# Kernel optimization log

Hardware: AMD Instinct MI355X
Metric: run time of the kernel (lower is better)

The kernel has to match this reference:

```python
import jax, jax.numpy as jnp
import numpy as np

B, M, N = 262144, 3, 256   # batch, soil layers, runoff features
H1, H2 = 256, 128          # MLP hidden widths (layer_units[:-1]); last layer is scalar


def setup_inputs() -> dict:
    key = jax.random.key(0)
    ks = jax.random.split(key, 9)
    runoff = jax.random.uniform(ks[0], (B, M, N), dtype=jnp.float32)
    last_flow = jax.random.uniform(ks[1], (B, M), dtype=jnp.float32)
    last_free_water = jax.random.uniform(ks[2], (B, M), dtype=jnp.float32)
    s = 0.05
    # m independent tiny MLPs, stacked along leading axis m
    W1 = jax.random.normal(ks[3], (M, N, H1), dtype=jnp.float32) * s
    b1 = jnp.zeros((M, H1), dtype=jnp.float32)
    W2 = jax.random.normal(ks[4], (M, H1, H2), dtype=jnp.float32) * s
    b2 = jnp.zeros((M, H2), dtype=jnp.float32)
    W3 = jax.random.normal(ks[5], (M, H2), dtype=jnp.float32) * s  # last layer has 1 unit
    b3 = jnp.zeros((M,), dtype=jnp.float32)
    return {
        "last_flow": last_flow,
        "last_free_water": last_free_water,
        "runoff": runoff,
        "W1": W1, "b1": b1, "W2": W2, "b2": b2, "W3": W3, "b3": b3,
    }


def reference(last_flow, last_free_water, runoff, W1, b1, W2, b2, W3, b3):
    # step 1: add summed runoff to free-water state  (B, M)
    free_water = last_free_water + jnp.sum(runoff, axis=-1)
    # step 2: m small MLPs -> per-layer outflow ratio in (0,1), batched over m via einsum
    a1 = jax.nn.relu(jnp.einsum('bmn,mnh->bmh', runoff, W1) + b1)        # (B, M, H1)
    a2 = jax.nn.relu(jnp.einsum('bmh,mhk->bmk', a1, W2) + b2)            # (B, M, H2)
    ratio = jax.nn.sigmoid(jnp.einsum('bmk,mk->bm', a2, W3) + b3)        # (B, M)
    # step 3: blend free water with previous flow
    flow = free_water * ratio + last_flow * (1.0 - ratio)
    # step 4: update free-water state
    new_free_water = free_water - flow
    return (new_free_water, flow)
```

## Files before the change

kernel.cpp:

```cpp
#include <hip/hip_runtime.h>
#include <hip/hip_bf16.h>


#define B_TOT 262144
#define M_    3
#define N_    256
#define H1_   256
#define H2_   128
#define BM_   (B_TOT * M_)

typedef __bf16 bf16_t;
typedef __bf16  bf16x8 __attribute__((ext_vector_type(8)));
typedef float   f32x16 __attribute__((ext_vector_type(16)));
typedef float   f32x4  __attribute__((ext_vector_type(4)));

__device__ __forceinline__ unsigned pack_bf2(float lo, float hi) {
  union { bf16_t b; unsigned short u; } a, c;
  a.b = (bf16_t)lo; c.b = (bf16_t)hi;
  return ((unsigned)c.u << 16) | (unsigned)a.u;
}

__device__ __forceinline__ void gload_lds16(const void* g, void* l) {
  __builtin_amdgcn_global_load_lds(
      (const __attribute__((address_space(1))) void*)g,
      (__attribute__((address_space(3))) void*)l, 16, 0, 0);
}

__global__ __launch_bounds__(256) void prep_weights(
    const float* __restrict__ W1, const float* __restrict__ W2,
    bf16_t* __restrict__ w1s, bf16_t* __restrict__ w2s)
{
  int id = blockIdx.x * 256 + threadIdx.x;
  const int NW1 = M_ * 16 * 8 * 64;
  const int NW2 = M_ * 16 * 4 * 64;
  if (id < NW1) {
    int lane = id & 63;
    int t    = (id >> 6) & 7;
    int kk   = (id >> 9) & 15;
    int m    = id >> 13;
    int h  = 32 * t + (lane & 31);
    int n0 = 16 * kk + 8 * (lane >> 5);
    bf16x8 v;
#pragma unroll
    for (int ii = 0; ii < 8; ++ii)
      v[ii] = (bf16_t)W1[((size_t)m * N_ + (n0 + ii)) * H1_ + h];
    *reinterpret_cast<bf16x8*>(&w1s[(size_t)id * 8]) = v;
  } else if (id < NW1 + NW2) {
    int j    = id - NW1;
    int lane = j & 63;
    int t2   = (j >> 6) & 3;
    int kk2  = (j >> 8) & 15;
    int m    = j >> 12;
    int k2 = 32 * t2 + (lane & 31);
    int h0 = 16 * kk2 + 8 * (lane >> 5);
    bf16x8 v;
#pragma unroll
    for (int ii = 0; ii < 8; ++ii)
      v[ii] = (bf16_t)W2[((size_t)m * H1_ + (h0 + ii)) * H2_ + k2];
    *reinterpret_cast<bf16x8*>(&w2s[(size_t)j * 8]) = v;
  }
}

__global__ __launch_bounds__(256, 2) void reservoir_kernel(
    const float* __restrict__ last_flow,
    const float* __restrict__ last_fw,
    const float* __restrict__ runoff,
    const float* __restrict__ b1,
    const float* __restrict__ b2,
    const float* __restrict__ W3,
    const float* __restrict__ b3,
    const bf16_t* __restrict__ w1s,
    const bf16_t* __restrict__ w2s,
    float* __restrict__ out)
{
  __shared__ alignas(16) bf16_t sW1[2][4096];
  __shared__ alignas(16) bf16_t sW2[2][2048];
  __shared__ alignas(16) float  sB1[H1_];
  __shared__ alignas(16) float  sB2[H2_];
  __shared__ alignas(16) float  sW3[H2_];

  const int tid  = threadIdx.x;
  const int lane = tid & 63;
  const int wv   = tid >> 6;
  const int m    = blockIdx.y;
  const int hi   = lane >> 5;
  const int r    = lane & 31;
  const int row  = blockIdx.x * 128 + wv * 32 + r;

  const bf16_t* w1base = w1s + (size_t)m * 65536;
  const bf16_t* w2base = w2s + (size_t)m * 32768;

  auto stage_w1 = [&](int kk, int buf) {
#pragma unroll
    for (int c = 0; c < 2; ++c) {
      int chunk = wv * 2 + c;
      gload_lds16(w1base + (size_t)kk * 4096 + chunk * 512 + lane * 8,
                  &sW1[buf][chunk * 512]);
    }
  };
  auto stage_w2 = [&](int kk2, int buf) {
    gload_lds16(w2base + (size_t)kk2 * 2048 + wv * 512 + lane * 8,
                &sW2[buf][wv * 512]);
  };

  if (tid < H1_) sB1[tid] = b1[m * H1_ + tid];
  if (tid < H2_) { sB2[tid] = b2[m * H2_ + tid]; sW3[tid] = W3[m * H2_ + tid]; }
  stage_w1(0, 0);
  __syncthreads();

  f32x16 acc1[8];
#pragma unroll
  for (int t = 0; t < 8; ++t) {
#pragma unroll
    for (int g2 = 0; g2 < 4; ++g2) {
      f32x4 bv = *reinterpret_cast<const f32x4*>(&sB1[32 * t + 8 * g2 + 4 * hi]);
      acc1[t][4 * g2 + 0] = bv[0];
      acc1[t][4 * g2 + 1] = bv[1];
      acc1[t][4 * g2 + 2] = bv[2];
      acc1[t][4 * g2 + 3] = bv[3];
    }
  }

  float rsum = 0.f;
  const float* rowptr = runoff + ((size_t)row * M_ + m) * N_;

#pragma unroll
  for (int kk = 0; kk < 16; ++kk) {
    const int cb = kk & 1;
    if (kk < 15) stage_w1(kk + 1, cb ^ 1);
    else         stage_w2(0, 0);

    f32x4 qa = *reinterpret_cast<const f32x4*>(&rowptr[16 * kk + 8 * hi]);
    f32x4 qb = *reinterpret_cast<const f32x4*>(&rowptr[16 * kk + 8 * hi + 4]);
    rsum += qa[0] + qa[1] + qa[2] + qa[3] + qb[0] + qb[1] + qb[2] + qb[3];
    bf16x8 bfrag;
    bfrag[0] = (bf16_t)qa[0]; bfrag[1] = (bf16_t)qa[1];
    bfrag[2] = (bf16_t)qa[2]; bfrag[3] = (bf16_t)qa[3];
    bfrag[4] = (bf16_t)qb[0]; bfrag[5] = (bf16_t)qb[1];
    bfrag[6] = (bf16_t)qb[2]; bfrag[7] = (bf16_t)qb[3];

#pragma unroll
    for (int t = 0; t < 8; ++t) {
      bf16x8 afrag = *reinterpret_cast<const bf16x8*>(&sW1[cb][t * 512 + lane * 8]);
      acc1[t] = __builtin_amdgcn_mfma_f32_32x32x16_bf16(afrag, bfrag, acc1[t], 0, 0, 0);
    }
    __syncthreads();
  }

  unsigned P[8][2][2][2];
#pragma unroll
  for (int t = 0; t < 8; ++t)
#pragma unroll
    for (int q = 0; q < 2; ++q)
#pragma unroll
      for (int v = 0; v < 2; ++v)
#pragma unroll
        for (int s = 0; s < 2; ++s) {
          int e = 8 * q + 4 * v + 2 * s;
          P[t][q][v][s] = pack_bf2(fmaxf(acc1[t][e], 0.f),
                                   fmaxf(acc1[t][e + 1], 0.f));
        }

  f32x16 acc2[4];
#pragma unroll
  for (int t2 = 0; t2 < 4; ++t2) {
#pragma unroll
    for (int g2 = 0; g2 < 4; ++g2) {
      f32x4 bv = *reinterpret_cast<const f32x4*>(&sB2[32 * t2 + 8 * g2 + 4 * hi]);
      acc2[t2][4 * g2 + 0] = bv[0];
      acc2[t2][4 * g2 + 1] = bv[1];
      acc2[t2][4 * g2 + 2] = bv[2];
      acc2[t2][4 * g2 + 3] = bv[3];
    }
  }

#pragma unroll
  for (int kk2 = 0; kk2 < 16; ++kk2) {
    const int cb = kk2 & 1;
    if (kk2 < 15) stage_w2(kk2 + 1, cb ^ 1);
    const int t = kk2 >> 1, q = kk2 & 1;

    auto r0 = __builtin_amdgcn_permlane32_swap(P[t][q][0][0], P[t][q][1][0], false, false);
    auto r1 = __builtin_amdgcn_permlane32_swap(P[t][q][0][1], P[t][q][1][1], false, false);
    union { unsigned u[4]; bf16x8 v; } bb;
    bb.u[0] = r0[0]; bb.u[1] = r1[0]; bb.u[2] = r0[1]; bb.u[3] = r1[1];

#pragma unroll
    for (int t2 = 0; t2 < 4; ++t2) {
      bf16x8 afrag = *reinterpret_cast<const bf16x8*>(&sW2[cb][t2 * 512 + lane * 8]);
      acc2[t2] = __builtin_amdgcn_mfma_f32_32x32x16_bf16(afrag, bb.v, acc2[t2], 0, 0, 0);
    }
    __syncthreads();
  }

  float part = 0.f;
#pragma unroll
  for (int t2 = 0; t2 < 4; ++t2) {
#pragma unroll
    for (int g2 = 0; g2 < 4; ++g2) {
      f32x4 w3v = *reinterpret_cast<const f32x4*>(&sW3[32 * t2 + 8 * g2 + 4 * hi]);
      part += fmaxf(acc2[t2][4 * g2 + 0], 0.f) * w3v[0]
            + fmaxf(acc2[t2][4 * g2 + 1], 0.f) * w3v[1]
            + fmaxf(acc2[t2][4 * g2 + 2], 0.f) * w3v[2]
            + fmaxf(acc2[t2][4 * g2 + 3], 0.f) * w3v[3];
    }
  }
  part += __shfl_xor(part, 32, 64);
  rsum += __shfl_xor(rsum, 32, 64);

  const float x     = part + b3[m];
  const float ratio = 1.0f / (1.0f + __expf(-x));
  const size_t oi   = (size_t)row * M_ + m;
  const float fw    = last_fw[oi] + rsum;
  const float lf    = last_flow[oi];
  const float flow  = fw * ratio + lf * (1.0f - ratio);
  if (hi == 0) {
    out[oi]        = fw - flow;
    out[BM_ + oi]  = flow;
  }
}

extern "C" void kernel_launch(void* const* d_in, const int* in_sizes, int n_in,
                              void* d_out, int out_size, void* d_ws, size_t ws_size,
                              hipStream_t stream) {
  const float* last_flow = (const float*)d_in[0];
  const float* last_fw   = (const float*)d_in[1];
  const float* runoff    = (const float*)d_in[2];
  const float* W1 = (const float*)d_in[3];
  const float* b1 = (const float*)d_in[4];
  const float* W2 = (const float*)d_in[5];
  const float* b2 = (const float*)d_in[6];
  const float* W3 = (const float*)d_in[7];
  const float* b3 = (const float*)d_in[8];
  float* out = (float*)d_out;

  bf16_t* w1s = (bf16_t*)d_ws;
  bf16_t* w2s = w1s + (size_t)M_ * 65536;

  prep_weights<<<144, 256, 0, stream>>>(W1, W2, w1s, w2s);

  dim3 grid(B_TOT / 128, M_);
  reservoir_kernel<<<grid, 256, 0, stream>>>(last_flow, last_fw, runoff,
                                             b1, b2, W3, b3, w1s, w2s, out);
}
```

Before: 326.8 us.

## Stage runoff tiles through swizzled LDS with async loads and double buffering

Runoff rows are now fetched with global_load_lds into a double-buffered, XOR-swizzled LDS tile, 32 columns per stage, instead of each lane doing direct strided global loads per k-step. W1 staging is widened to two k-steps per stage, halving the number of barriers in layer 1. This is meant to coalesce runoff reads, overlap them with MFMA work and cut synchronisation. The cost is roughly 64KB of LDS per block, which may reduce occupancy below the two blocks per CU requested by the launch bounds.

```diff
diff --git a/kernel.cpp b/kernel.cpp
--- a/kernel.cpp
+++ b/kernel.cpp
@@ -73,7 +73,8 @@
     const bf16_t* __restrict__ w2s,
     float* __restrict__ out)
 {
-  __shared__ alignas(16) bf16_t sW1[2][4096];
+  __shared__ alignas(16) float  sR[2][128 * 32];
+  __shared__ alignas(16) bf16_t sW1[2][8192];
   __shared__ alignas(16) bf16_t sW2[2][2048];
   __shared__ alignas(16) float  sB1[H1_];
   __shared__ alignas(16) float  sB2[H2_];
@@ -85,16 +86,30 @@
   const int m    = blockIdx.y;
   const int hi   = lane >> 5;
   const int r    = lane & 31;
-  const int row  = blockIdx.x * 128 + wv * 32 + r;
+  const int r7   = r & 7;
+  const int row0 = blockIdx.x * 128;
+  const int row  = row0 + wv * 32 + r;
+
+  const int l3 = lane >> 3;
+  const int gsw = (lane & 7) ^ l3;
 
   const bf16_t* w1base = w1s + (size_t)m * 65536;
   const bf16_t* w2base = w2s + (size_t)m * 32768;
 
-  auto stage_w1 = [&](int kk, int buf) {
-#pragma unroll
-    for (int c = 0; c < 2; ++c) {
-      int chunk = wv * 2 + c;
-      gload_lds16(w1base + (size_t)kk * 4096 + chunk * 512 + lane * 8,
+  auto stage_R = [&](int g, int buf) {
+#pragma unroll
+    for (int c = 0; c < 4; ++c) {
+      int slab = wv * 4 + c;
+      const float* src = runoff
+          + ((size_t)(row0 + slab * 8 + l3) * M_ + m) * N_ + 32 * g + 4 * gsw;
+      gload_lds16(src, &sR[buf][slab * 256]);
+    }
+  };
+  auto stage_w1g = [&](int g, int buf) {
+#pragma unroll
+    for (int c = 0; c < 4; ++c) {
+      int chunk = wv * 4 + c;
+      gload_lds16(w1base + (size_t)g * 8192 + chunk * 512 + lane * 8,
                   &sW1[buf][chunk * 512]);
     }
   };
@@ -103,9 +118,10 @@
                 &sW2[buf][wv * 512]);
   };
 
-  if (tid < H1_) sB1[tid] = b1[m * H1_ + tid];
+  sB1[tid] = b1[m * H1_ + tid];
   if (tid < H2_) { sB2[tid] = b2[m * H2_ + tid]; sW3[tid] = W3[m * H2_ + tid]; }
-  stage_w1(0, 0);
+  stage_R(0, 0);
+  stage_w1g(0, 0);
   __syncthreads();
 
   f32x16 acc1[8];
@@ -122,27 +138,32 @@
   }
 
   float rsum = 0.f;
-  const float* rowptr = runoff + ((size_t)row * M_ + m) * N_;
-
-#pragma unroll
-  for (int kk = 0; kk < 16; ++kk) {
-    const int cb = kk & 1;
-    if (kk < 15) stage_w1(kk + 1, cb ^ 1);
-    else         stage_w2(0, 0);
-
-    f32x4 qa = *reinterpret_cast<const f32x4*>(&rowptr[16 * kk + 8 * hi]);
-    f32x4 qb = *reinterpret_cast<const f32x4*>(&rowptr[16 * kk + 8 * hi + 4]);
-    rsum += qa[0] + qa[1] + qa[2] + qa[3] + qb[0] + qb[1] + qb[2] + qb[3];
-    bf16x8 bfrag;
-    bfrag[0] = (bf16_t)qa[0]; bfrag[1] = (bf16_t)qa[1];
-    bfrag[2] = (bf16_t)qa[2]; bfrag[3] = (bf16_t)qa[3];
-    bfrag[4] = (bf16_t)qb[0]; bfrag[5] = (bf16_t)qb[1];
-    bfrag[6] = (bf16_t)qb[2]; bfrag[7] = (bf16_t)qb[3];
-
-#pragma unroll
-    for (int t = 0; t < 8; ++t) {
-      bf16x8 afrag = *reinterpret_cast<const bf16x8*>(&sW1[cb][t * 512 + lane * 8]);
-      acc1[t] = __builtin_amdgcn_mfma_f32_32x32x16_bf16(afrag, bfrag, acc1[t], 0, 0, 0);
+  const float* rrow_base_off = nullptr; (void)rrow_base_off;
+
+#pragma unroll
+  for (int g = 0; g < 8; ++g) {
+    const int cb = g & 1;
+    if (g < 7) { stage_R(g + 1, cb ^ 1); stage_w1g(g + 1, cb ^ 1); }
+    else       { stage_w2(0, 0); }
+
+#pragma unroll
+    for (int q = 0; q < 2; ++q) {
+      const float* rb = &sR[cb][(wv * 32 + r) * 32];
+      f32x4 qa = *reinterpret_cast<const f32x4*>(&rb[((4 * q + 2 * hi + 0) ^ r7) * 4]);
+      f32x4 qb = *reinterpret_cast<const f32x4*>(&rb[((4 * q + 2 * hi + 1) ^ r7) * 4]);
+      rsum += qa[0] + qa[1] + qa[2] + qa[3] + qb[0] + qb[1] + qb[2] + qb[3];
+      bf16x8 bfrag;
+      bfrag[0] = (bf16_t)qa[0]; bfrag[1] = (bf16_t)qa[1];
+      bfrag[2] = (bf16_t)qa[2]; bfrag[3] = (bf16_t)qa[3];
+      bfrag[4] = (bf16_t)qb[0]; bfrag[5] = (bf16_t)qb[1];
+      bfrag[6] = (bf16_t)qb[2]; bfrag[7] = (bf16_t)qb[3];
+
+#pragma unroll
+      for (int t = 0; t < 8; ++t) {
+        bf16x8 afrag = *reinterpret_cast<const bf16x8*>(
+            &sW1[cb][q * 4096 + t * 512 + lane * 8]);
+        acc1[t] = __builtin_amdgcn_mfma_f32_32x32x16_bf16(afrag, bfrag, acc1[t], 0, 0, 0);
+      }
     }
     __syncthreads();
   }
@@ -187,7 +208,8 @@
 
 #pragma unroll
     for (int t2 = 0; t2 < 4; ++t2) {
-      bf16x8 afrag = *reinterpret_cast<const bf16x8*>(&sW2[cb][t2 * 512 + lane * 8]);
+      bf16x8 afrag = *reinterpret_cast<const bf16x8*>(
+          &sW2[cb][t2 * 512 + lane * 8]);
       acc2[t2] = __builtin_amdgcn_mfma_f32_32x32x16_bf16(afrag, bb.v, acc2[t2], 0, 0, 0);
     }
     __syncthreads();
```

Measured after the change: 289.1 us. 11.5% less time.

## Make MLP kernel persistent with LDS-staged activations and prefetched runoff tiles

Applied to the files above, without the earlier changes.

Restructures the kernel into 768 persistent blocks that each loop over eight 128-row tiles. Runoff is converted to bf16 and staged in swizzled LDS, with the next tile's global loads interleaved with the current tile's layer-1 MFMAs. Weight fragments are now read straight from global memory (L2) with register prefetch instead of LDS staging. The hidden layer goes through LDS for layer 2. The runoff sum is now computed from bf16-rounded values, which reduces its precision.

```diff
diff --git a/kernel.cpp b/kernel.cpp
--- a/kernel.cpp
+++ b/kernel.cpp
@@ -18,12 +18,6 @@
   union { bf16_t b; unsigned short u; } a, c;
   a.b = (bf16_t)lo; c.b = (bf16_t)hi;
   return ((unsigned)c.u << 16) | (unsigned)a.u;
-}
-
-__device__ __forceinline__ void gload_lds16(const void* g, void* l) {
-  __builtin_amdgcn_global_load_lds(
-      (const __attribute__((address_space(1))) void*)g,
-      (__attribute__((address_space(3))) void*)l, 16, 0, 0);
 }
 
 __global__ __launch_bounds__(256) void prep_weights(
@@ -61,7 +55,7 @@
   }
 }
 
-__global__ __launch_bounds__(256, 2) void reservoir_kernel(
+__global__ __launch_bounds__(256, 1) void reservoir_kernel(
     const float* __restrict__ last_flow,
     const float* __restrict__ last_fw,
     const float* __restrict__ runoff,
@@ -73,151 +67,206 @@
     const bf16_t* __restrict__ w2s,
     float* __restrict__ out)
 {
-  __shared__ alignas(16) bf16_t sW1[2][4096];
-  __shared__ alignas(16) bf16_t sW2[2][2048];
-  __shared__ alignas(16) float  sB1[H1_];
-  __shared__ alignas(16) float  sB2[H2_];
-  __shared__ alignas(16) float  sW3[H2_];
+  __shared__ alignas(16) bf16_t sX[128 * 256];
+  __shared__ alignas(16) bf16_t sY[128 * 256];
+  __shared__ alignas(16) float  sB1f[H1_];
+  __shared__ alignas(16) float  sB2f[H2_];
+  __shared__ alignas(16) float  sW3f[H2_];
+  __shared__ alignas(16) float  sPart[4][128];
+  __shared__ alignas(16) float  sRsum[128];
 
   const int tid  = threadIdx.x;
   const int lane = tid & 63;
   const int wv   = tid >> 6;
-  const int m    = blockIdx.y;
   const int hi   = lane >> 5;
   const int r    = lane & 31;
-  const int row  = blockIdx.x * 128 + wv * 32 + r;
+
+  const int m        = blockIdx.x >> 8;
+  const size_t rbase = (size_t)(blockIdx.x & 255) * 1024;
 
   const bf16_t* w1base = w1s + (size_t)m * 65536;
   const bf16_t* w2base = w2s + (size_t)m * 32768;
-
-  auto stage_w1 = [&](int kk, int buf) {
-#pragma unroll
-    for (int c = 0; c < 2; ++c) {
-      int chunk = wv * 2 + c;
-      gload_lds16(w1base + (size_t)kk * 4096 + chunk * 512 + lane * 8,
-                  &sW1[buf][chunk * 512]);
-    }
-  };
-  auto stage_w2 = [&](int kk2, int buf) {
-    gload_lds16(w2base + (size_t)kk2 * 2048 + wv * 512 + lane * 8,
-                &sW2[buf][wv * 512]);
-  };
-
-  if (tid < H1_) sB1[tid] = b1[m * H1_ + tid];
-  if (tid < H2_) { sB2[tid] = b2[m * H2_ + tid]; sW3[tid] = W3[m * H2_ + tid]; }
-  stage_w1(0, 0);
+  const float   b3v    = b3[m];
+
+  sB1f[tid] = b1[m * H1_ + tid];
+  if (tid < H2_) { sB2f[tid] = b2[m * H2_ + tid]; sW3f[tid] = W3[m * H2_ + tid]; }
+
+  f32x4 tmp[8];
+  uint2 pkbuf[4][8];
+
+#define STAGE_LOAD(grp, nu) {                                                 \
+    size_t gb = rbase + (size_t)(nu) * 128 + wv * 32 + (grp) * 8;             \
+    _Pragma("unroll")                                                         \
+    for (int j = 0; j < 8; ++j)                                               \
+      tmp[j] = *reinterpret_cast<const f32x4*>(                               \
+          runoff + ((gb + j) * M_ + m) * N_ + lane * 4);                      \
+  }
+#define STAGE_PACK(grp) {                                                     \
+    _Pragma("unroll")                                                         \
+    for (int j = 0; j < 8; ++j) {                                             \
+      pkbuf[grp][j].x = pack_bf2(tmp[j][0], tmp[j][1]);                       \
+      pkbuf[grp][j].y = pack_bf2(tmp[j][2], tmp[j][3]);                       \
+    }                                                                         \
+  }
+#define STAGE_WRITE_ALL() {                                                   \
+    _Pragma("unroll")                                                         \
+    for (int g2 = 0; g2 < 4; ++g2) {                                          \
+      _Pragma("unroll")                                                       \
+      for (int j = 0; j < 8; ++j) {                                           \
+        int prow = wv * 32 + g2 * 8 + j;                                      \
+        int p8   = lane ^ ((prow & 15) << 1);                                 \
+        *reinterpret_cast<uint2*>(&sX[prow * 256 + p8 * 4]) = pkbuf[g2][j];   \
+      }                                                                       \
+    }                                                                         \
+  }
+
+#pragma unroll
+  for (int g2 = 0; g2 < 4; ++g2) { STAGE_LOAD(g2, 0); STAGE_PACK(g2); }
+  STAGE_WRITE_ALL();
   __syncthreads();
 
-  f32x16 acc1[8];
-#pragma unroll
-  for (int t = 0; t < 8; ++t) {
-#pragma unroll
-    for (int g2 = 0; g2 < 4; ++g2) {
-      f32x4 bv = *reinterpret_cast<const f32x4*>(&sB1[32 * t + 8 * g2 + 4 * hi]);
-      acc1[t][4 * g2 + 0] = bv[0];
-      acc1[t][4 * g2 + 1] = bv[1];
-      acc1[t][4 * g2 + 2] = bv[2];
-      acc1[t][4 * g2 + 3] = bv[3];
-    }
-  }
-
-  float rsum = 0.f;
-  const float* rowptr = runoff + ((size_t)row * M_ + m) * N_;
-
-#pragma unroll
-  for (int kk = 0; kk < 16; ++kk) {
-    const int cb = kk & 1;
-    if (kk < 15) stage_w1(kk + 1, cb ^ 1);
-    else         stage_w2(0, 0);
-
-    f32x4 qa = *reinterpret_cast<const f32x4*>(&rowptr[16 * kk + 8 * hi]);
-    f32x4 qb = *reinterpret_cast<const f32x4*>(&rowptr[16 * kk + 8 * hi + 4]);
-    rsum += qa[0] + qa[1] + qa[2] + qa[3] + qb[0] + qb[1] + qb[2] + qb[3];
-    bf16x8 bfrag;
-    bfrag[0] = (bf16_t)qa[0]; bfrag[1] = (bf16_t)qa[1];
-    bfrag[2] = (bf16_t)qa[2]; bfrag[3] = (bf16_t)qa[3];
-    bfrag[4] = (bf16_t)qb[0]; bfrag[5] = (bf16_t)qb[1];
-    bfrag[6] = (bf16_t)qb[2]; bfrag[7] = (bf16_t)qb[3];
-
-#pragma unroll
-    for (int t = 0; t < 8; ++t) {
-      bf16x8 afrag = *reinterpret_cast<const bf16x8*>(&sW1[cb][t * 512 + lane * 8]);
-      acc1[t] = __builtin_amdgcn_mfma_f32_32x32x16_bf16(afrag, bfrag, acc1[t], 0, 0, 0);
-    }
+  for (int u = 0; u < 8; ++u) {
+    f32x16 acc1[2][4];
+#pragma unroll
+    for (int t = 0; t < 2; ++t)
+#pragma unroll
+      for (int rg = 0; rg < 4; ++rg)
+        acc1[t][rg] = f32x16{};
+
+    float rsum = 0.f;
+    bf16x8 afc0 = *reinterpret_cast<const bf16x8*>(
+        w1base + 0 * 4096 + (2 * wv + 0) * 512 + lane * 8);
+    bf16x8 afc1 = *reinterpret_cast<const bf16x8*>(
+        w1base + 0 * 4096 + (2 * wv + 1) * 512 + lane * 8);
+
+#define L1_STEP(kk) {                                                         \
+    bf16x8 afn0{}, afn1{};                                                    \
+    if ((kk) < 15) {                                                          \
+      afn0 = *reinterpret_cast<const bf16x8*>(                                \
+          w1base + ((kk) + 1) * 4096 + (2 * wv + 0) * 512 + lane * 8);        \
+      afn1 = *reinterpret_cast<const bf16x8*>(                                \
+          w1base + ((kk) + 1) * 4096 + (2 * wv + 1) * 512 + lane * 8);        \
+    }                                                                         \
+    _Pragma("unroll")                                                         \
+    for (int rg = 0; rg < 4; ++rg) {                                          \
+      bf16x8 bf = *reinterpret_cast<const bf16x8*>(                           \
+          &sX[(rg * 32 + r) * 256 + (((2 * (kk) + hi) ^ (r & 15)) * 8)]);     \
+      if (rg == wv) {                                                         \
+        _Pragma("unroll")                                                     \
+        for (int j = 0; j < 8; ++j) rsum += (float)bf[j];                     \
+      }                                                                       \
+      acc1[0][rg] = __builtin_amdgcn_mfma_f32_32x32x16_bf16(afc0, bf, acc1[0][rg], 0, 0, 0); \
+      acc1[1][rg] = __builtin_amdgcn_mfma_f32_32x32x16_bf16(afc1, bf, acc1[1][rg], 0, 0, 0); \
+    }                                                                         \
+    afc0 = afn0; afc1 = afn1;                                                 \
+  }
+
+    if (u < 7) { STAGE_LOAD(0, u + 1); }
+    L1_STEP(0)  L1_STEP(1)  L1_STEP(2)  L1_STEP(3)
+    if (u < 7) { STAGE_PACK(0); STAGE_LOAD(1, u + 1); }
+    L1_STEP(4)  L1_STEP(5)  L1_STEP(6)  L1_STEP(7)
+    if (u < 7) { STAGE_PACK(1); STAGE_LOAD(2, u + 1); }
+    L1_STEP(8)  L1_STEP(9)  L1_STEP(10) L1_STEP(11)
+    if (u < 7) { STAGE_PACK(2); STAGE_LOAD(3, u + 1); }
+    L1_STEP(12) L1_STEP(13) L1_STEP(14) L1_STEP(15)
+    if (u < 7) { STAGE_PACK(3); }
+
+    rsum += __shfl_xor(rsum, 32, 64);
+
     __syncthreads();
-  }
-
-  unsigned P[8][2][2][2];
-#pragma unroll
-  for (int t = 0; t < 8; ++t)
-#pragma unroll
-    for (int q = 0; q < 2; ++q)
-#pragma unroll
-      for (int v = 0; v < 2; ++v)
-#pragma unroll
-        for (int s = 0; s < 2; ++s) {
-          int e = 8 * q + 4 * v + 2 * s;
-          P[t][q][v][s] = pack_bf2(fmaxf(acc1[t][e], 0.f),
-                                   fmaxf(acc1[t][e + 1], 0.f));
+
+    if (u < 7) STAGE_WRITE_ALL();
+    if (hi == 0) sRsum[wv * 32 + r] = rsum;
+
+#pragma unroll
+    for (int t = 0; t < 2; ++t) {
+      float2 b1p[8];
+#pragma unroll
+      for (int j = 0; j < 8; ++j) {
+        int hl = 2 * (j & 1) + 8 * (j >> 1) + 4 * hi;
+        b1p[j] = *reinterpret_cast<const float2*>(&sB1f[wv * 64 + t * 32 + hl]);
+      }
+#pragma unroll
+      for (int rg = 0; rg < 4; ++rg) {
+#pragma unroll
+        for (int j = 0; j < 8; ++j) {
+          int hl = 2 * (j & 1) + 8 * (j >> 1) + 4 * hi;
+          int h  = wv * 64 + t * 32 + hl;
+          unsigned val = pack_bf2(fmaxf(acc1[t][rg][2 * j]     + b1p[j].x, 0.f),
+                                  fmaxf(acc1[t][rg][2 * j + 1] + b1p[j].y, 0.f));
+          int row = rg * 32 + r;
+          *reinterpret_cast<unsigned*>(
+              &sY[row * 256 + (((h >> 3) ^ (row & 15)) * 8 + (h & 7))]) = val;
         }
-
-  f32x16 acc2[4];
-#pragma unroll
-  for (int t2 = 0; t2 < 4; ++t2) {
-#pragma unroll
-    for (int g2 = 0; g2 < 4; ++g2) {
-      f32x4 bv = *reinterpret_cast<const f32x4*>(&sB2[32 * t2 + 8 * g2 + 4 * hi]);
-      acc2[t2][4 * g2 + 0] = bv[0];
-      acc2[t2][4 * g2 + 1] = bv[1];
-      acc2[t2][4 * g2 + 2] = bv[2];
-      acc2[t2][4 * g2 + 3] = bv[3];
-    }
-  }
-
-#pragma unroll
-  for (int kk2 = 0; kk2 < 16; ++kk2) {
-    const int cb = kk2 & 1;
-    if (kk2 < 15) stage_w2(kk2 + 1, cb ^ 1);
-    const int t = kk2 >> 1, q = kk2 & 1;
-
-    auto r0 = __builtin_amdgcn_permlane32_swap(P[t][q][0][0], P[t][q][1][0], false, false);
-    auto r1 = __builtin_amdgcn_permlane32_swap(P[t][q][0][1], P[t][q][1][1], false, false);
-    union { unsigned u[4]; bf16x8 v; } bb;
-    bb.u[0] = r0[0]; bb.u[1] = r1[0]; bb.u[2] = r0[1]; bb.u[3] = r1[1];
-
-#pragma unroll
-    for (int t2 = 0; t2 < 4; ++t2) {
-      bf16x8 afrag = *reinterpret_cast<const bf16x8*>(&sW2[cb][t2 * 512 + lane * 8]);
-      acc2[t2] = __builtin_amdgcn_mfma_f32_32x32x16_bf16(afrag, bb.v, acc2[t2], 0, 0, 0);
-    }
+      }
+    }
+
     __syncthreads();
-  }
-
-  float part = 0.f;
-#pragma unroll
-  for (int t2 = 0; t2 < 4; ++t2) {
-#pragma unroll
-    for (int g2 = 0; g2 < 4; ++g2) {
-      f32x4 w3v = *reinterpret_cast<const f32x4*>(&sW3[32 * t2 + 8 * g2 + 4 * hi]);
-      part += fmaxf(acc2[t2][4 * g2 + 0], 0.f) * w3v[0]
-            + fmaxf(acc2[t2][4 * g2 + 1], 0.f) * w3v[1]
-            + fmaxf(acc2[t2][4 * g2 + 2], 0.f) * w3v[2]
-            + fmaxf(acc2[t2][4 * g2 + 3], 0.f) * w3v[3];
-    }
-  }
-  part += __shfl_xor(part, 32, 64);
-  rsum += __shfl_xor(rsum, 32, 64);
-
-  const float x     = part + b3[m];
-  const float ratio = 1.0f / (1.0f + __expf(-x));
-  const size_t oi   = (size_t)row * M_ + m;
-  const float fw    = last_fw[oi] + rsum;
-  const float lf    = last_flow[oi];
-  const float flow  = fw * ratio + lf * (1.0f - ratio);
-  if (hi == 0) {
-    out[oi]        = fw - flow;
-    out[BM_ + oi]  = flow;
-  }
+
+    f32x16 acc2[4];
+#pragma unroll
+    for (int rg = 0; rg < 4; ++rg) acc2[rg] = f32x16{};
+
+    bf16x8 wfc = *reinterpret_cast<const bf16x8*>(
+        w2base + 0 * 2048 + wv * 512 + lane * 8);
+
+#define L2_STEP(kk2) {                                                        \
+    bf16x8 wfn{};                                                             \
+    if ((kk2) < 15)                                                           \
+      wfn = *reinterpret_cast<const bf16x8*>(                                 \
+          w2base + ((kk2) + 1) * 2048 + wv * 512 + lane * 8);                 \
+    _Pragma("unroll")                                                         \
+    for (int rg = 0; rg < 4; ++rg) {                                          \
+      bf16x8 bf = *reinterpret_cast<const bf16x8*>(                           \
+          &sY[(rg * 32 + r) * 256 + (((2 * (kk2) + hi) ^ (r & 15)) * 8)]);    \
+      acc2[rg] = __builtin_amdgcn_mfma_f32_32x32x16_bf16(wfc, bf, acc2[rg], 0, 0, 0); \
+    }                                                                         \
+    wfc = wfn;                                                                \
+  }
+
+    L2_STEP(0)  L2_STEP(1)  L2_STEP(2)  L2_STEP(3)
+    L2_STEP(4)  L2_STEP(5)  L2_STEP(6)  L2_STEP(7)
+    L2_STEP(8)  L2_STEP(9)  L2_STEP(10) L2_STEP(11)
+    L2_STEP(12) L2_STEP(13) L2_STEP(14) L2_STEP(15)
+
+    float b2r[16], w3r[16];
+#pragma unroll
+    for (int e = 0; e < 16; ++e) {
+      int k2 = wv * 32 + (e & 3) + 8 * (e >> 2) + 4 * hi;
+      b2r[e] = sB2f[k2];
+      w3r[e] = sW3f[k2];
+    }
+#pragma unroll
+    for (int rg = 0; rg < 4; ++rg) {
+      float part = 0.f;
+#pragma unroll
+      for (int e = 0; e < 16; ++e)
+        part += fmaxf(acc2[rg][e] + b2r[e], 0.f) * w3r[e];
+      part += __shfl_xor(part, 32, 64);
+      if (hi == 0) sPart[wv][rg * 32 + r] = part;
+    }
+
+    __syncthreads();
+
+    if (tid < 128) {
+      const size_t grow = rbase + (size_t)u * 128 + tid;
+      const size_t oi   = grow * M_ + m;
+      const float pt    = sPart[0][tid] + sPart[1][tid] + sPart[2][tid]
+                        + sPart[3][tid] + b3v;
+      const float ratio = 1.0f / (1.0f + __expf(-pt));
+      const float fw    = last_fw[oi] + sRsum[tid];
+      const float lf    = last_flow[oi];
+      const float flow  = fw * ratio + lf * (1.0f - ratio);
+      out[oi]       = fw - flow;
+      out[BM_ + oi] = flow;
+    }
+  }
+
+#undef STAGE_LOAD
+#undef STAGE_PACK
+#undef STAGE_WRITE_ALL
+#undef L1_STEP
+#undef L2_STEP
 }
 
 extern "C" void kernel_launch(void* const* d_in, const int* in_sizes, int n_in,
@@ -239,7 +288,6 @@
 
   prep_weights<<<144, 256, 0, stream>>>(W1, W2, w1s, w2s);
 
-  dim3 grid(B_TOT / 128, M_);
-  reservoir_kernel<<<grid, 256, 0, stream>>>(last_flow, last_fw, runoff,
-                                             b1, b2, W3, b3, w1s, w2s, out);
-}
+  reservoir_kernel<<<768, 256, 0, stream>>>(last_flow, last_fw, runoff,
+                                            b1, b2, W3, b3, w1s, w2s, out);
+}
```

Result: slower. 505.6 us (+54.7%).

## Split hidden units across waves with LDS-staged activations and per-block row loop

Applied to the files above, without the earlier changes.

Restructures the MLP kernel so each block handles 256 rows of one soil layer in 8 chunks of 32. Runoff is staged into swizzled LDS as bf16, each wave computes a slice of the hidden units, and layer-2 inputs are exchanged through LDS. Weights are now read directly from global memory (L2) instead of double-buffered LDS staging. The goal is lower register pressure for higher occupancy (launch bounds 4) and less weight traffic per row. It adds several syncs per chunk, and the rowsum now comes from bf16-rounded values, which slightly changes precision.

```diff
diff --git a/kernel.cpp b/kernel.cpp
--- a/kernel.cpp
+++ b/kernel.cpp
@@ -18,12 +18,6 @@
   union { bf16_t b; unsigned short u; } a, c;
   a.b = (bf16_t)lo; c.b = (bf16_t)hi;
   return ((unsigned)c.u << 16) | (unsigned)a.u;
-}
-
-__device__ __forceinline__ void gload_lds16(const void* g, void* l) {
-  __builtin_amdgcn_global_load_lds(
-      (const __attribute__((address_space(1))) void*)g,
-      (__attribute__((address_space(3))) void*)l, 16, 0, 0);
 }
 
 __global__ __launch_bounds__(256) void prep_weights(
@@ -61,7 +55,7 @@
   }
 }
 
-__global__ __launch_bounds__(256, 2) void reservoir_kernel(
+__global__ __launch_bounds__(256, 4) void reservoir_kernel(
     const float* __restrict__ last_flow,
     const float* __restrict__ last_fw,
     const float* __restrict__ runoff,
@@ -73,150 +67,121 @@
     const bf16_t* __restrict__ w2s,
     float* __restrict__ out)
 {
-  __shared__ alignas(16) bf16_t sW1[2][4096];
-  __shared__ alignas(16) bf16_t sW2[2][2048];
-  __shared__ alignas(16) float  sB1[H1_];
-  __shared__ alignas(16) float  sB2[H2_];
-  __shared__ alignas(16) float  sW3[H2_];
+  __shared__ alignas(16) bf16_t sR[32 * 256];
+  __shared__ alignas(16) bf16_t sY[32 * 256];
+  __shared__ alignas(16) float  sB1f[H1_];
+  __shared__ alignas(16) float  sB2f[H2_];
+  __shared__ alignas(16) float  sW3f[H2_];
+  __shared__ alignas(16) float  sPart[4][32];
+  __shared__ alignas(16) float  sRsum[32];
 
   const int tid  = threadIdx.x;
   const int lane = tid & 63;
   const int wv   = tid >> 6;
-  const int m    = blockIdx.y;
   const int hi   = lane >> 5;
   const int r    = lane & 31;
-  const int row  = blockIdx.x * 128 + wv * 32 + r;
+  const int r15  = r & 15;
+
+  const int m        = blockIdx.x % 3;
+  const size_t rbase = (size_t)(blockIdx.x / 3) * 256;
 
   const bf16_t* w1base = w1s + (size_t)m * 65536;
   const bf16_t* w2base = w2s + (size_t)m * 32768;
-
-  auto stage_w1 = [&](int kk, int buf) {
-#pragma unroll
-    for (int c = 0; c < 2; ++c) {
-      int chunk = wv * 2 + c;
-      gload_lds16(w1base + (size_t)kk * 4096 + chunk * 512 + lane * 8,
-                  &sW1[buf][chunk * 512]);
-    }
-  };
-  auto stage_w2 = [&](int kk2, int buf) {
-    gload_lds16(w2base + (size_t)kk2 * 2048 + wv * 512 + lane * 8,
-                &sW2[buf][wv * 512]);
-  };
-
-  if (tid < H1_) sB1[tid] = b1[m * H1_ + tid];
-  if (tid < H2_) { sB2[tid] = b2[m * H2_ + tid]; sW3[tid] = W3[m * H2_ + tid]; }
-  stage_w1(0, 0);
-  __syncthreads();
-
-  f32x16 acc1[8];
-#pragma unroll
-  for (int t = 0; t < 8; ++t) {
-#pragma unroll
-    for (int g2 = 0; g2 < 4; ++g2) {
-      f32x4 bv = *reinterpret_cast<const f32x4*>(&sB1[32 * t + 8 * g2 + 4 * hi]);
-      acc1[t][4 * g2 + 0] = bv[0];
-      acc1[t][4 * g2 + 1] = bv[1];
-      acc1[t][4 * g2 + 2] = bv[2];
-      acc1[t][4 * g2 + 3] = bv[3];
-    }
-  }
-
-  float rsum = 0.f;
-  const float* rowptr = runoff + ((size_t)row * M_ + m) * N_;
-
-#pragma unroll
-  for (int kk = 0; kk < 16; ++kk) {
-    const int cb = kk & 1;
-    if (kk < 15) stage_w1(kk + 1, cb ^ 1);
-    else         stage_w2(0, 0);
-
-    f32x4 qa = *reinterpret_cast<const f32x4*>(&rowptr[16 * kk + 8 * hi]);
-    f32x4 qb = *reinterpret_cast<const f32x4*>(&rowptr[16 * kk + 8 * hi + 4]);
-    rsum += qa[0] + qa[1] + qa[2] + qa[3] + qb[0] + qb[1] + qb[2] + qb[3];
-    bf16x8 bfrag;
-    bfrag[0] = (bf16_t)qa[0]; bfrag[1] = (bf16_t)qa[1];
-    bfrag[2] = (bf16_t)qa[2]; bfrag[3] = (bf16_t)qa[3];
-    bfrag[4] = (bf16_t)qb[0]; bfrag[5] = (bf16_t)qb[1];
-    bfrag[6] = (bf16_t)qb[2]; bfrag[7] = (bf16_t)qb[3];
-
-#pragma unroll
-    for (int t = 0; t < 8; ++t) {
-      bf16x8 afrag = *reinterpret_cast<const bf16x8*>(&sW1[cb][t * 512 + lane * 8]);
-      acc1[t] = __builtin_amdgcn_mfma_f32_32x32x16_bf16(afrag, bfrag, acc1[t], 0, 0, 0);
+  const float   b3v    = b3[m];
+
+  sB1f[tid] = b1[m * H1_ + tid];
+  if (tid < H2_) { sB2f[tid] = b2[m * H2_ + tid]; sW3f[tid] = W3[m * H2_ + tid]; }
+
+  for (int u = 0; u < 8; ++u) {
+    {
+      const float* src = runoff
+          + ((rbase + u * 32 + wv * 8) * M_ + m) * N_ + lane * 4;
+#pragma unroll
+      for (int j = 0; j < 8; ++j) {
+        f32x4 v = *reinterpret_cast<const f32x4*>(src + (size_t)j * (M_ * N_));
+        uint2 d;
+        d.x = pack_bf2(v[0], v[1]);
+        d.y = pack_bf2(v[2], v[3]);
+        const int rl = wv * 8 + j;
+        const int p8 = lane ^ ((rl & 15) << 1);
+        *reinterpret_cast<uint2*>(&sR[rl * 256 + p8 * 4]) = d;
+      }
     }
     __syncthreads();
-  }
-
-  unsigned P[8][2][2][2];
-#pragma unroll
-  for (int t = 0; t < 8; ++t)
-#pragma unroll
-    for (int q = 0; q < 2; ++q)
-#pragma unroll
-      for (int v = 0; v < 2; ++v)
-#pragma unroll
-        for (int s = 0; s < 2; ++s) {
-          int e = 8 * q + 4 * v + 2 * s;
-          P[t][q][v][s] = pack_bf2(fmaxf(acc1[t][e], 0.f),
-                                   fmaxf(acc1[t][e + 1], 0.f));
-        }
-
-  f32x16 acc2[4];
-#pragma unroll
-  for (int t2 = 0; t2 < 4; ++t2) {
-#pragma unroll
-    for (int g2 = 0; g2 < 4; ++g2) {
-      f32x4 bv = *reinterpret_cast<const f32x4*>(&sB2[32 * t2 + 8 * g2 + 4 * hi]);
-      acc2[t2][4 * g2 + 0] = bv[0];
-      acc2[t2][4 * g2 + 1] = bv[1];
-      acc2[t2][4 * g2 + 2] = bv[2];
-      acc2[t2][4 * g2 + 3] = bv[3];
-    }
-  }
-
-#pragma unroll
-  for (int kk2 = 0; kk2 < 16; ++kk2) {
-    const int cb = kk2 & 1;
-    if (kk2 < 15) stage_w2(kk2 + 1, cb ^ 1);
-    const int t = kk2 >> 1, q = kk2 & 1;
-
-    auto r0 = __builtin_amdgcn_permlane32_swap(P[t][q][0][0], P[t][q][1][0], false, false);
-    auto r1 = __builtin_amdgcn_permlane32_swap(P[t][q][0][1], P[t][q][1][1], false, false);
-    union { unsigned u[4]; bf16x8 v; } bb;
-    bb.u[0] = r0[0]; bb.u[1] = r1[0]; bb.u[2] = r0[1]; bb.u[3] = r1[1];
-
-#pragma unroll
-    for (int t2 = 0; t2 < 4; ++t2) {
-      bf16x8 afrag = *reinterpret_cast<const bf16x8*>(&sW2[cb][t2 * 512 + lane * 8]);
-      acc2[t2] = __builtin_amdgcn_mfma_f32_32x32x16_bf16(afrag, bb.v, acc2[t2], 0, 0, 0);
+
+    f32x16 acc1[2] = {f32x16{}, f32x16{}};
+    float rsum = 0.f;
+#pragma unroll
+    for (int kk = 0; kk < 16; ++kk) {
+      bf16x8 bf = *reinterpret_cast<const bf16x8*>(
+          &sR[r * 256 + (((2 * kk + hi) ^ r15) * 8)]);
+      if (wv == 0) {
+#pragma unroll
+        for (int j = 0; j < 8; ++j) rsum += (float)bf[j];
+      }
+#pragma unroll
+      for (int tl = 0; tl < 2; ++tl) {
+        bf16x8 af = *reinterpret_cast<const bf16x8*>(
+            w1base + (size_t)kk * 4096 + (2 * wv + tl) * 512 + lane * 8);
+        acc1[tl] = __builtin_amdgcn_mfma_f32_32x32x16_bf16(af, bf, acc1[tl], 0, 0, 0);
+      }
+    }
+
+#pragma unroll
+    for (int tl = 0; tl < 2; ++tl) {
+      const int tg = 2 * wv + tl;
+#pragma unroll
+      for (int g2 = 0; g2 < 4; ++g2) {
+        const int hb = 32 * tg + 8 * g2 + 4 * hi;
+        f32x4 bv = *reinterpret_cast<const f32x4*>(&sB1f[hb]);
+        uint2 d;
+        d.x = pack_bf2(fmaxf(acc1[tl][4 * g2 + 0] + bv[0], 0.f),
+                       fmaxf(acc1[tl][4 * g2 + 1] + bv[1], 0.f));
+        d.y = pack_bf2(fmaxf(acc1[tl][4 * g2 + 2] + bv[2], 0.f),
+                       fmaxf(acc1[tl][4 * g2 + 3] + bv[3], 0.f));
+        const int G = 4 * tg + g2;
+        *reinterpret_cast<uint2*>(
+            &sY[r * 256 + ((G ^ r15) * 8) + hi * 4]) = d;
+      }
+    }
+    if (wv == 0) {
+      rsum += __shfl_xor(rsum, 32, 64);
+      if (hi == 0) sRsum[r] = rsum;
     }
     __syncthreads();
-  }
-
-  float part = 0.f;
-#pragma unroll
-  for (int t2 = 0; t2 < 4; ++t2) {
-#pragma unroll
-    for (int g2 = 0; g2 < 4; ++g2) {
-      f32x4 w3v = *reinterpret_cast<const f32x4*>(&sW3[32 * t2 + 8 * g2 + 4 * hi]);
-      part += fmaxf(acc2[t2][4 * g2 + 0], 0.f) * w3v[0]
-            + fmaxf(acc2[t2][4 * g2 + 1], 0.f) * w3v[1]
-            + fmaxf(acc2[t2][4 * g2 + 2], 0.f) * w3v[2]
-            + fmaxf(acc2[t2][4 * g2 + 3], 0.f) * w3v[3];
-    }
-  }
-  part += __shfl_xor(part, 32, 64);
-  rsum += __shfl_xor(rsum, 32, 64);
-
-  const float x     = part + b3[m];
-  const float ratio = 1.0f / (1.0f + __expf(-x));
-  const size_t oi   = (size_t)row * M_ + m;
-  const float fw    = last_fw[oi] + rsum;
-  const float lf    = last_flow[oi];
-  const float flow  = fw * ratio + lf * (1.0f - ratio);
-  if (hi == 0) {
-    out[oi]        = fw - flow;
-    out[BM_ + oi]  = flow;
+
+    f32x16 acc2 = f32x16{};
+#pragma unroll
+    for (int kk2 = 0; kk2 < 16; ++kk2) {
+      bf16x8 bf = *reinterpret_cast<const bf16x8*>(
+          &sY[r * 256 + (((2 * kk2 + hi) ^ r15) * 8)]);
+      bf16x8 wf = *reinterpret_cast<const bf16x8*>(
+          w2base + (size_t)kk2 * 2048 + wv * 512 + lane * 8);
+      acc2 = __builtin_amdgcn_mfma_f32_32x32x16_bf16(wf, bf, acc2, 0, 0, 0);
+    }
+
+    float part = 0.f;
+#pragma unroll
+    for (int e = 0; e < 16; ++e) {
+      const int k2 = 32 * wv + (e & 3) + 8 * (e >> 2) + 4 * hi;
+      part += fmaxf(acc2[e] + sB2f[k2], 0.f) * sW3f[k2];
+    }
+    part += __shfl_xor(part, 32, 64);
+    if (hi == 0) sPart[wv][r] = part;
+    __syncthreads();
+
+    if (tid < 32) {
+      const size_t grow = rbase + u * 32 + tid;
+      const size_t oi   = grow * M_ + m;
+      const float pt    = sPart[0][tid] + sPart[1][tid] + sPart[2][tid]
+                        + sPart[3][tid] + b3v;
+      const float ratio = 1.0f / (1.0f + __expf(-pt));
+      const float fw    = last_fw[oi] + sRsum[tid];
+      const float lf    = last_flow[oi];
+      const float flow  = fw * ratio + lf * (1.0f - ratio);
+      out[oi]       = fw - flow;
+      out[BM_ + oi] = flow;
+    }
   }
 }
 
@@ -239,7 +204,6 @@
 
   prep_weights<<<144, 256, 0, stream>>>(W1, W2, w1s, w2s);
 
-  dim3 grid(B_TOT / 128, M_);
-  reservoir_kernel<<<grid, 256, 0, stream>>>(last_flow, last_fw, runoff,
+  reservoir_kernel<<<3072, 256, 0, stream>>>(last_flow, last_fw, runoff,
                                              b1, b2, W3, b3, w1s, w2s, out);
 }
```

After: 971.7 us. 2.97x slower.
